# Kernel tuning notes

Hardware: AMD Instinct MI355X
Metric: run time of the kernel (lower is better)

## Reference

```python
import jax, jax.numpy as jnp
import numpy as np


def _overlap_add_fft_conv(signal, kernel):
    """Vectorized overlap-add FFT convolution.

    signal: (B, K, T) float; kernel: (B, K, R) float.
    Returns (B, K, T), identical math to the torch per-block loop (the
    ortho-normed rfft/irfft pair on the signal cancels, kernel rfft uses
    default backward norm, exactly as in the original code).
    """
    B, K, T = signal.shape
    R = kernel.shape[-1]
    fft_len = 2 << (R - 1).bit_length()          # e.g. R=4000 -> 8192
    step = fft_len - R + 1                        # hop between blocks
    pad_len = (-T) % step                         # pad T up to multiple of step
    L = T + pad_len
    n_blocks = L // step

    # split padded signal into non-overlapping blocks, zero-pad each to fft_len
    sig = jnp.pad(signal, ((0, 0), (0, 0), (0, pad_len)))
    blocks = sig.reshape(B, K, n_blocks, step)
    blocks = jnp.pad(blocks, ((0, 0), (0, 0), (0, 0), (0, fft_len - step)))

    kernel_fft = jnp.fft.rfft(
        jnp.pad(kernel, ((0, 0), (0, 0), (0, fft_len - R))))      # (B,K,F)
    block_fft = jnp.fft.rfft(blocks, norm='ortho')                # (B,K,n_blocks,F)
    conv = jnp.fft.irfft(block_fft * kernel_fft[:, :, None, :],
                         norm='ortho')                            # (B,K,n_blocks,fft_len)

    # overlap-add: block i contributes at offset i*step, length fft_len
    idx = jnp.arange(n_blocks)[:, None] * step + jnp.arange(fft_len)[None, :]
    out = jnp.zeros((B, K, L + R - 1), dtype=conv.dtype)
    out = out.at[:, :, idx].add(conv)
    return out[:, :, :T]


def setup_inputs() -> dict:
    key = jax.random.key(0)
    k1, k2 = jax.random.split(key)
    onsets = jax.random.normal(k1, (8, 8, 262144), dtype=jnp.float32)
    sources = jax.random.normal(k2, (8, 8, 4000), dtype=jnp.float32)
    return {"onsets": onsets, "sources": sources, "delay_compensation": 0}


def reference(onsets, sources, delay_compensation):
    # delay_compensation is unused in the original module as well
    return _overlap_add_fft_conv(onsets, sources)
```

## Files before the change

kernel.cpp:

```cpp
#include <hip/hip_runtime.h>

#define T_LEN 262144
#define R_LEN 4000
#define NCH 64
#define NCHUNK 253
#define NSLOT 4624
#define LDS_BYTES 73984

typedef __attribute__((ext_vector_type(8))) short bf16x8;
typedef __attribute__((ext_vector_type(16))) float f32x16;

static __device__ __forceinline__ unsigned short f2bf(float f) {
  unsigned u = __builtin_bit_cast(unsigned, f);
  unsigned r = 0x7FFFu + ((u >> 16) & 1u);
  return (unsigned short)((u + r) >> 16);
}

__global__ __launch_bounds__(256) void build_btf(const float* __restrict__ src,
                                                 unsigned short* __restrict__ btf) {
  int t0 = blockIdx.x * 256 + threadIdx.x;
  if (t0 >= NCH * NCHUNK * 64) return;
  int lane = t0 & 63;
  int t = (t0 >> 6) % NCHUNK;
  int ch = t0 / (64 * NCHUNK);
  int j = lane & 31;
  int h = lane >> 5;
  int kbase = 4000 + j - 16 * t - 8 * h;
  const float* k = src + (size_t)ch * R_LEN;
  unsigned short vals[8];
#pragma unroll
  for (int e = 0; e < 8; ++e) {
    int r = kbase - e;
    float f = (r >= 0 && r < R_LEN) ? k[r] : 0.0f;
    vals[e] = f2bf(f);
  }
  unsigned int* dst = (unsigned int*)(btf + (size_t)t0 * 8);
  dst[0] = (unsigned int)vals[0] | ((unsigned int)vals[1] << 16);
  dst[1] = (unsigned int)vals[2] | ((unsigned int)vals[3] << 16);
  dst[2] = (unsigned int)vals[4] | ((unsigned int)vals[5] << 16);
  dst[3] = (unsigned int)vals[6] | ((unsigned int)vals[7] << 16);
}

__global__ __launch_bounds__(512, 4) void conv_main(const float* __restrict__ x,
                                                    const unsigned short* __restrict__ btf,
                                                    float* __restrict__ out) {
  __shared__ alignas(16) unsigned char xs[LDS_BYTES];
  const int bid = blockIdx.x;
  const int ch = bid & 63;
  const int T0 = (bid >> 6) << 15;
  const float* xch = x + (size_t)ch * T_LEN;

  for (int n = threadIdx.x; n < NSLOT; n += 512) {
    int pb = n >> 1;
    int r = pb / 289;
    int q = pb - 289 * r;
    int s = 2 * (8 * q + r) + (n & 1);
    int gi = T0 - 4000 + 8 * s;
    float v0, v1, v2, v3, v4, v5, v6, v7;
    if (gi >= 0 && gi + 8 <= T_LEN) {
      float4 a = *(const float4*)(xch + gi);
      float4 b = *(const float4*)(xch + gi + 4);
      v0 = a.x; v1 = a.y; v2 = a.z; v3 = a.w;
      v4 = b.x; v5 = b.y; v6 = b.z; v7 = b.w;
    } else {
      v0 = (gi + 0 >= 0 && gi + 0 < T_LEN) ? xch[gi + 0] : 0.f;
      v1 = (gi + 1 >= 0 && gi + 1 < T_LEN) ? xch[gi + 1] : 0.f;
      v2 = (gi + 2 >= 0 && gi + 2 < T_LEN) ? xch[gi + 2] : 0.f;
      v3 = (gi + 3 >= 0 && gi + 3 < T_LEN) ? xch[gi + 3] : 0.f;
      v4 = (gi + 4 >= 0 && gi + 4 < T_LEN) ? xch[gi + 4] : 0.f;
      v5 = (gi + 5 >= 0 && gi + 5 < T_LEN) ? xch[gi + 5] : 0.f;
      v6 = (gi + 6 >= 0 && gi + 6 < T_LEN) ? xch[gi + 6] : 0.f;
      v7 = (gi + 7 >= 0 && gi + 7 < T_LEN) ? xch[gi + 7] : 0.f;
    }
    uint4 pk;
    pk.x = (unsigned int)f2bf(v0) | ((unsigned int)f2bf(v1) << 16);
    pk.y = (unsigned int)f2bf(v2) | ((unsigned int)f2bf(v3) << 16);
    pk.z = (unsigned int)f2bf(v4) | ((unsigned int)f2bf(v5) << 16);
    pk.w = (unsigned int)f2bf(v6) | ((unsigned int)f2bf(v7) << 16);
    *(uint4*)(xs + 16 * n) = pk;
  }
  __syncthreads();

  const int lane = threadIdx.x & 63;
  const int w = threadIdx.x >> 6;
  const int i = lane & 31;
  const int h = lane >> 5;
  const int lanepart = 32 * i + 16 * h;
  const char* bbase = (const char*)btf + ((size_t)ch * NCHUNK) * 1024 + (size_t)lane * 16;

  auto aread = [&](int q) -> bf16x8 {
    int b0 = 256 * w + q;
    int addr = (((b0 >> 3) + (b0 & 7) * 289) << 5) + lanepart;
    return *(const bf16x8*)(xs + addr);
  };
  auto bload = [&](int t) -> bf16x8 {
    int tc = t > 252 ? 252 : t;
    return *(const bf16x8*)(bbase + (size_t)tc * 1024);
  };

  f32x16 acc[4] = {};
  bf16x8 zero8 = {};
  bf16x8 E0 = bload(0), E1 = zero8, E2 = zero8, E3 = zero8;
  bf16x8 O0 = bload(1), O1 = zero8, O2 = zero8, O3 = zero8;
  bf16x8 a = aread(0);

#define DO_STEP(B0, B1, B2, B3, QQ)                                                      \
  {                                                                                      \
    bf16x8 nb = bload((QQ) + 2);                                                         \
    bf16x8 an = aread((QQ) + 1);                                                         \
    acc[0] = __builtin_amdgcn_mfma_f32_32x32x16_bf16(a, B0, acc[0], 0, 0, 0);            \
    acc[1] = __builtin_amdgcn_mfma_f32_32x32x16_bf16(a, B1, acc[1], 0, 0, 0);            \
    acc[2] = __builtin_amdgcn_mfma_f32_32x32x16_bf16(a, B2, acc[2], 0, 0, 0);            \
    acc[3] = __builtin_amdgcn_mfma_f32_32x32x16_bf16(a, B3, acc[3], 0, 0, 0);            \
    B3 = B2; B2 = B1; B1 = B0; B0 = nb;                                                  \
    a = an;                                                                              \
  }

#pragma unroll 4
  for (int q = 0; q < 258; q += 2) {
    DO_STEP(E0, E1, E2, E3, q);
    DO_STEP(O0, O1, O2, O3, q + 1);
  }
#undef DO_STEP

  float* och = out + (size_t)ch * T_LEN + T0 + 4096 * w;
#pragma unroll
  for (int c = 0; c < 4; ++c) {
#pragma unroll
    for (int r = 0; r < 16; ++r) {
      int row = (r & 3) + 8 * (r >> 2) + 4 * h;
      och[32 * c + 128 * row + i] = acc[c][r];
    }
  }
}

extern "C" void kernel_launch(void* const* d_in, const int* in_sizes, int n_in,
                              void* d_out, int out_size, void* d_ws, size_t ws_size,
                              hipStream_t stream) {
  const float* onsets  = (const float*)d_in[0];
  const float* sources = (const float*)d_in[1];
  unsigned short* btf  = (unsigned short*)d_ws;
  float* out = (float*)d_out;

  int nthr = NCH * NCHUNK * 64;
  build_btf<<<(nthr + 255) / 256, 256, 0, stream>>>(sources, btf);
  conv_main<<<512, 512, 0, stream>>>(onsets, btf, out);
}
```

Measured before the change: 122.3 us.

## Stage filter B-fragments through an LDS ring buffer with per-phase barriers

The convolution kernel stops loading the Toeplitz B fragments directly from global memory inside the MFMA loop. They now go into a double-buffered LDS ring: each wave prefetches two chunks per phase into registers, stores them after the MFMAs, and a block barrier ends each phase. Blocks are halved to 256 threads covering 16K samples, launched as 1024 blocks, and A reads get a deeper prefetch. This aims to take global-load latency off the MFMA critical path, at the cost of 32 barriers per block and more LDS traffic.

```diff
diff --git a/kernel.cpp b/kernel.cpp
--- a/kernel.cpp
+++ b/kernel.cpp
@@ -4,8 +4,13 @@
 #define R_LEN 4000
 #define NCH 64
 #define NCHUNK 253
-#define NSLOT 4624
-#define LDS_BYTES 73984
+#define PERM_C 161
+#define NBLK 1288
+#define A_BYTES (NBLK * 32)
+#define NSLOT (NBLK * 2)
+#define RING_OFF A_BYTES
+#define LDS_BYTES (A_BYTES + 16384)
+#define NPHASE 32
 
 typedef __attribute__((ext_vector_type(8))) short bf16x8;
 typedef __attribute__((ext_vector_type(16))) float f32x16;
@@ -41,19 +46,24 @@
   dst[3] = (unsigned int)vals[6] | ((unsigned int)vals[7] << 16);
 }
 
-__global__ __launch_bounds__(512, 4) void conv_main(const float* __restrict__ x,
+__global__ __launch_bounds__(256, 2) void conv_main(const float* __restrict__ x,
                                                     const unsigned short* __restrict__ btf,
                                                     float* __restrict__ out) {
   __shared__ alignas(16) unsigned char xs[LDS_BYTES];
   const int bid = blockIdx.x;
   const int ch = bid & 63;
-  const int T0 = (bid >> 6) << 15;
+  const int T0 = (bid >> 6) << 14;
   const float* xch = x + (size_t)ch * T_LEN;
+  const char* btc = (const char*)btf + (size_t)ch * NCHUNK * 1024;
 
-  for (int n = threadIdx.x; n < NSLOT; n += 512) {
+  const int tid = threadIdx.x;
+  const int lane = tid & 63;
+  const int w = tid >> 6;
+
+  for (int n = tid; n < NSLOT; n += 256) {
     int pb = n >> 1;
-    int r = pb / 289;
-    int q = pb - 289 * r;
+    int r = pb / PERM_C;
+    int q = pb - PERM_C * r;
     int s = 2 * (8 * q + r) + (n & 1);
     int gi = T0 - 4000 + 8 * s;
     float v0, v1, v2, v3, v4, v5, v6, v7;
@@ -79,47 +89,71 @@
     pk.w = (unsigned int)f2bf(v6) | ((unsigned int)f2bf(v7) << 16);
     *(uint4*)(xs + 16 * n) = pk;
   }
+
+#pragma unroll
+  for (int g = 0; g < 2; ++g) {
+#pragma unroll
+    for (int k = 0; k < 2; ++k) {
+      int t = 8 * g + 2 * w + k;
+      uint4 r = *(const uint4*)(btc + (size_t)t * 1024 + lane * 16);
+      *(uint4*)(xs + RING_OFF + g * 8192 + (2 * w + k) * 1024 + lane * 16) = r;
+    }
+  }
   __syncthreads();
 
-  const int lane = threadIdx.x & 63;
-  const int w = threadIdx.x >> 6;
   const int i = lane & 31;
   const int h = lane >> 5;
   const int lanepart = 32 * i + 16 * h;
-  const char* bbase = (const char*)btf + ((size_t)ch * NCHUNK) * 1024 + (size_t)lane * 16;
 
   auto aread = [&](int q) -> bf16x8 {
     int b0 = 256 * w + q;
-    int addr = (((b0 >> 3) + (b0 & 7) * 289) << 5) + lanepart;
+    int addr = (((b0 >> 3) + (b0 & 7) * PERM_C) << 5) + lanepart;
     return *(const bf16x8*)(xs + addr);
   };
-  auto bload = [&](int t) -> bf16x8 {
-    int tc = t > 252 ? 252 : t;
-    return *(const bf16x8*)(bbase + (size_t)tc * 1024);
+  auto ldsB = [&](int t) -> bf16x8 {
+    return *(const bf16x8*)(xs + RING_OFF + ((t >> 3) & 1) * 8192 + (t & 7) * 1024 + lane * 16);
   };
 
   f32x16 acc[4] = {};
   bf16x8 zero8 = {};
-  bf16x8 E0 = bload(0), E1 = zero8, E2 = zero8, E3 = zero8;
-  bf16x8 O0 = bload(1), O1 = zero8, O2 = zero8, O3 = zero8;
-  bf16x8 a = aread(0);
+  bf16x8 E0 = ldsB(0), E1 = zero8, E2 = zero8, E3 = zero8;
+  bf16x8 O0 = ldsB(1), O1 = zero8, O2 = zero8, O3 = zero8;
+  bf16x8 a_cur = aread(0), a_n1 = aread(1);
 
 #define DO_STEP(B0, B1, B2, B3, QQ)                                                      \
   {                                                                                      \
-    bf16x8 nb = bload((QQ) + 2);                                                         \
-    bf16x8 an = aread((QQ) + 1);                                                         \
-    acc[0] = __builtin_amdgcn_mfma_f32_32x32x16_bf16(a, B0, acc[0], 0, 0, 0);            \
-    acc[1] = __builtin_amdgcn_mfma_f32_32x32x16_bf16(a, B1, acc[1], 0, 0, 0);            \
-    acc[2] = __builtin_amdgcn_mfma_f32_32x32x16_bf16(a, B2, acc[2], 0, 0, 0);            \
-    acc[3] = __builtin_amdgcn_mfma_f32_32x32x16_bf16(a, B3, acc[3], 0, 0, 0);            \
+    bf16x8 nb = ldsB((QQ) + 2);                                                          \
+    bf16x8 a2 = aread((QQ) + 2);                                                         \
+    acc[0] = __builtin_amdgcn_mfma_f32_32x32x16_bf16(a_cur, B0, acc[0], 0, 0, 0);        \
+    acc[1] = __builtin_amdgcn_mfma_f32_32x32x16_bf16(a_cur, B1, acc[1], 0, 0, 0);        \
+    acc[2] = __builtin_amdgcn_mfma_f32_32x32x16_bf16(a_cur, B2, acc[2], 0, 0, 0);        \
+    acc[3] = __builtin_amdgcn_mfma_f32_32x32x16_bf16(a_cur, B3, acc[3], 0, 0, 0);        \
     B3 = B2; B2 = B1; B1 = B0; B0 = nb;                                                  \
-    a = an;                                                                              \
+    a_cur = a_n1; a_n1 = a2;                                                             \
   }
 
-#pragma unroll 4
-  for (int q = 0; q < 258; q += 2) {
-    DO_STEP(E0, E1, E2, E3, q);
-    DO_STEP(O0, O1, O2, O3, q + 1);
+#pragma unroll
+  for (int ii = 0; ii < 3; ++ii) {
+    DO_STEP(E0, E1, E2, E3, 2 * ii);
+    DO_STEP(O0, O1, O2, O3, 2 * ii + 1);
+  }
+
+  for (int p = 0; p < NPHASE; ++p) {
+    int gt = 8 * (p + 2) + 2 * w;
+    int t0c = gt > 252 ? 252 : gt;
+    int t1c = gt + 1 > 252 ? 252 : gt + 1;
+    uint4 r0 = *(const uint4*)(btc + (size_t)t0c * 1024 + lane * 16);
+    uint4 r1 = *(const uint4*)(btc + (size_t)t1c * 1024 + lane * 16);
+    int qb = 6 + 8 * p;
+#pragma unroll
+    for (int ii = 0; ii < 4; ++ii) {
+      DO_STEP(E0, E1, E2, E3, qb + 2 * ii);
+      DO_STEP(O0, O1, O2, O3, qb + 2 * ii + 1);
+    }
+    char* dst = (char*)xs + RING_OFF + (p & 1) * 8192 + 2 * w * 1024 + lane * 16;
+    *(uint4*)dst = r0;
+    *(uint4*)(dst + 1024) = r1;
+    __syncthreads();
   }
 #undef DO_STEP
 
@@ -144,5 +178,5 @@
 
   int nthr = NCH * NCHUNK * 64;
   build_btf<<<(nthr + 255) / 256, 256, 0, stream>>>(sources, btf);
-  conv_main<<<512, 512, 0, stream>>>(onsets, btf, out);
+  conv_main<<<1024, 256, 0, stream>>>(onsets, btf, out);
 }
```

Result: faster. 118.8 us (-2.9%).

## Widen per-wave output tile to 8 MFMA accumulators with new LDS signal layout

Applied to the files above, without the earlier changes.

Each wave now keeps 8 accumulator tiles instead of 4 and slides 8 Toeplitz B fragments, so each A fragment read from LDS feeds twice as many MFMAs. The block shrinks to 256 threads, each wave covering 8192 outputs. The LDS signal layout becomes a simpler transposed stride-145 scheme to avoid bank conflicts, and s_setprio wraps the MFMA bursts. The cost is many more live registers (8 f32x16 accumulators plus 16 B fragments), which lowers occupancy, and extra wasted steps at the edges.

```diff
diff --git a/kernel.cpp b/kernel.cpp
--- a/kernel.cpp
+++ b/kernel.cpp
@@ -4,8 +4,10 @@
 #define R_LEN 4000
 #define NCH 64
 #define NCHUNK 253
-#define NSLOT 4624
-#define LDS_BYTES 73984
+#define WBLK 4616
+#define SIG_M 145
+#define LDS_BYTES 74240
+#define NSTEP 272
 
 typedef __attribute__((ext_vector_type(8))) short bf16x8;
 typedef __attribute__((ext_vector_type(16))) float f32x16;
@@ -41,7 +43,7 @@
   dst[3] = (unsigned int)vals[6] | ((unsigned int)vals[7] << 16);
 }
 
-__global__ __launch_bounds__(512, 4) void conv_main(const float* __restrict__ x,
+__global__ __launch_bounds__(256, 2) void conv_main(const float* __restrict__ x,
                                                     const unsigned short* __restrict__ btf,
                                                     float* __restrict__ out) {
   __shared__ alignas(16) unsigned char xs[LDS_BYTES];
@@ -49,13 +51,14 @@
   const int ch = bid & 63;
   const int T0 = (bid >> 6) << 15;
   const float* xch = x + (size_t)ch * T_LEN;
+  const char* btc = (const char*)btf + (size_t)ch * NCHUNK * 1024;
 
-  for (int n = threadIdx.x; n < NSLOT; n += 512) {
-    int pb = n >> 1;
-    int r = pb / 289;
-    int q = pb - 289 * r;
-    int s = 2 * (8 * q + r) + (n & 1);
-    int gi = T0 - 4000 + 8 * s;
+  const int tid = threadIdx.x;
+  const int lane = tid & 63;
+  const int w = tid >> 6;
+
+  for (int n = tid; n < WBLK; n += 256) {
+    int gi = T0 - 4000 + 8 * n;
     float v0, v1, v2, v3, v4, v5, v6, v7;
     if (gi >= 0 && gi + 8 <= T_LEN) {
       float4 a = *(const float4*)(xch + gi);
@@ -77,59 +80,64 @@
     pk.y = (unsigned int)f2bf(v2) | ((unsigned int)f2bf(v3) << 16);
     pk.z = (unsigned int)f2bf(v4) | ((unsigned int)f2bf(v5) << 16);
     pk.w = (unsigned int)f2bf(v6) | ((unsigned int)f2bf(v7) << 16);
-    *(uint4*)(xs + 16 * n) = pk;
+    int sig = (n >> 5) + SIG_M * (n & 31);
+    *(uint4*)(xs + 16 * sig) = pk;
   }
   __syncthreads();
 
-  const int lane = threadIdx.x & 63;
-  const int w = threadIdx.x >> 6;
-  const int i = lane & 31;
+  const int l31 = lane & 31;
   const int h = lane >> 5;
-  const int lanepart = 32 * i + 16 * h;
-  const char* bbase = (const char*)btf + ((size_t)ch * NCHUNK) * 1024 + (size_t)lane * 16;
+  const unsigned abase = 16u * (32 * w + l31 + SIG_M * h);
 
   auto aread = [&](int q) -> bf16x8 {
-    int b0 = 256 * w + q;
-    int addr = (((b0 >> 3) + (b0 & 7) * 289) << 5) + lanepart;
-    return *(const bf16x8*)(xs + addr);
+    unsigned off = 16u * ((unsigned)(q >> 4) + 290u * (unsigned)(q & 15));
+    return *(const bf16x8*)(xs + abase + off);
   };
-  auto bload = [&](int t) -> bf16x8 {
+  auto bloadc = [&](int t) -> bf16x8 {
     int tc = t > 252 ? 252 : t;
-    return *(const bf16x8*)(bbase + (size_t)tc * 1024);
+    return *(const bf16x8*)(btc + (size_t)tc * 1024 + lane * 16);
   };
 
-  f32x16 acc[4] = {};
+  f32x16 acc[8] = {};
   bf16x8 zero8 = {};
-  bf16x8 E0 = bload(0), E1 = zero8, E2 = zero8, E3 = zero8;
-  bf16x8 O0 = bload(1), O1 = zero8, O2 = zero8, O3 = zero8;
-  bf16x8 a = aread(0);
+  bf16x8 E0 = bloadc(0), E1 = zero8, E2 = zero8, E3 = zero8,
+         E4 = zero8, E5 = zero8, E6 = zero8, E7 = zero8;
+  bf16x8 O0 = bloadc(1), O1 = zero8, O2 = zero8, O3 = zero8,
+         O4 = zero8, O5 = zero8, O6 = zero8, O7 = zero8;
+  bf16x8 a_cur = aread(0);
 
-#define DO_STEP(B0, B1, B2, B3, QQ)                                                      \
+#define DO_STEP(R0, R1, R2, R3, R4, R5, R6, R7, QQ)                                      \
   {                                                                                      \
-    bf16x8 nb = bload((QQ) + 2);                                                         \
+    bf16x8 nb = bloadc((QQ) + 2);                                                        \
     bf16x8 an = aread((QQ) + 1);                                                         \
-    acc[0] = __builtin_amdgcn_mfma_f32_32x32x16_bf16(a, B0, acc[0], 0, 0, 0);            \
-    acc[1] = __builtin_amdgcn_mfma_f32_32x32x16_bf16(a, B1, acc[1], 0, 0, 0);            \
-    acc[2] = __builtin_amdgcn_mfma_f32_32x32x16_bf16(a, B2, acc[2], 0, 0, 0);            \
-    acc[3] = __builtin_amdgcn_mfma_f32_32x32x16_bf16(a, B3, acc[3], 0, 0, 0);            \
-    B3 = B2; B2 = B1; B1 = B0; B0 = nb;                                                  \
-    a = an;                                                                              \
+    __builtin_amdgcn_s_setprio(1);                                                       \
+    acc[0] = __builtin_amdgcn_mfma_f32_32x32x16_bf16(a_cur, R0, acc[0], 0, 0, 0);        \
+    acc[1] = __builtin_amdgcn_mfma_f32_32x32x16_bf16(a_cur, R1, acc[1], 0, 0, 0);        \
+    acc[2] = __builtin_amdgcn_mfma_f32_32x32x16_bf16(a_cur, R2, acc[2], 0, 0, 0);        \
+    acc[3] = __builtin_amdgcn_mfma_f32_32x32x16_bf16(a_cur, R3, acc[3], 0, 0, 0);        \
+    acc[4] = __builtin_amdgcn_mfma_f32_32x32x16_bf16(a_cur, R4, acc[4], 0, 0, 0);        \
+    acc[5] = __builtin_amdgcn_mfma_f32_32x32x16_bf16(a_cur, R5, acc[5], 0, 0, 0);        \
+    acc[6] = __builtin_amdgcn_mfma_f32_32x32x16_bf16(a_cur, R6, acc[6], 0, 0, 0);        \
+    acc[7] = __builtin_amdgcn_mfma_f32_32x32x16_bf16(a_cur, R7, acc[7], 0, 0, 0);        \
+    __builtin_amdgcn_s_setprio(0);                                                       \
+    R7 = R6; R6 = R5; R5 = R4; R4 = R3; R3 = R2; R2 = R1; R1 = R0; R0 = nb;              \
+    a_cur = an;                                                                          \
   }
 
-#pragma unroll 4
-  for (int q = 0; q < 258; q += 2) {
-    DO_STEP(E0, E1, E2, E3, q);
-    DO_STEP(O0, O1, O2, O3, q + 1);
+#pragma unroll 8
+  for (int q = 0; q < NSTEP; q += 2) {
+    DO_STEP(E0, E1, E2, E3, E4, E5, E6, E7, q);
+    DO_STEP(O0, O1, O2, O3, O4, O5, O6, O7, q + 1);
   }
 #undef DO_STEP
 
-  float* och = out + (size_t)ch * T_LEN + T0 + 4096 * w;
+  float* och = out + (size_t)ch * T_LEN + T0 + 8192 * w;
 #pragma unroll
-  for (int c = 0; c < 4; ++c) {
+  for (int c = 0; c < 8; ++c) {
 #pragma unroll
     for (int r = 0; r < 16; ++r) {
-      int row = (r & 3) + 8 * (r >> 2) + 4 * h;
-      och[32 * c + 128 * row + i] = acc[c][r];
+      int irow = (r & 3) + 8 * (r >> 2) + 4 * h;
+      och[256 * irow + 32 * c + l31] = acc[c][r];
     }
   }
 }
@@ -144,5 +152,5 @@
 
   int nthr = NCH * NCHUNK * 64;
   build_btf<<<(nthr + 255) / 256, 256, 0, stream>>>(sources, btf);
-  conv_main<<<512, 512, 0, stream>>>(onsets, btf, out);
+  conv_main<<<512, 256, 0, stream>>>(onsets, btf, out);
 }
```

Result: faster. 118.0 us (-3.6%).
